# Kernel tuning notes

Hardware: AMD Instinct MI355X
Metric: run time of the kernel (lower is better)

The kernel has to match this reference:

```python
import jax, jax.numpy as jnp
import numpy as np

N_NODES = 100000
N_EDGES = 1600000
D = 128          # in_dim == out_dim
H = 8            # num_heads
DH = D // H      # head dim = 16
DFF = 2 * D
EPS_LN = 1e-5


def _ln(x, g, b):
    mu = jnp.mean(x, axis=-1, keepdims=True)
    var = jnp.var(x, axis=-1, keepdims=True)
    return (x - mu) * jax.lax.rsqrt(var + EPS_LN) * g + b


def setup_inputs() -> dict:
    key = jax.random.key(0)
    ks = jax.random.split(key, 12)
    s = 1.0 / np.sqrt(D)
    inp = {
        "h": jax.random.normal(ks[0], (N_NODES, D), jnp.float32),
        "src": jax.random.randint(ks[1], (N_EDGES,), 0, N_NODES, jnp.int32),
        "dst": jax.random.randint(ks[2], (N_EDGES,), 0, N_NODES, jnp.int32),
        "Wq": jax.random.normal(ks[3], (D, D), jnp.float32) * s,
        "Wk": jax.random.normal(ks[4], (D, D), jnp.float32) * s,
        "Wv": jax.random.normal(ks[5], (D, D), jnp.float32) * s,
        "Wo": jax.random.normal(ks[6], (D, D), jnp.float32) * s,
        "bo": jnp.zeros((D,), jnp.float32),
        "ln1_g": jnp.ones((D,), jnp.float32),
        "ln1_b": jnp.zeros((D,), jnp.float32),
        "W1": jax.random.normal(ks[7], (D, DFF), jnp.float32) * s,
        "b1": jnp.zeros((DFF,), jnp.float32),
        "W2": jax.random.normal(ks[8], (DFF, D), jnp.float32) * (1.0 / np.sqrt(DFF)),
        "b2": jnp.zeros((D,), jnp.float32),
        "ln2_g": jnp.ones((D,), jnp.float32),
        "ln2_b": jnp.zeros((D,), jnp.float32),
    }
    return inp


def reference(h, src, dst, Wq, Wk, Wv, Wo, bo, ln1_g, ln1_b, W1, b1, W2, b2, ln2_g, ln2_b):
    n = h.shape[0]
    # Q/K/V projections (no bias), split into heads: [N, H, DH]
    Q = (h @ Wq).reshape(n, H, DH)
    K = (h @ Wk).reshape(n, H, DH)
    V = (h @ Wv).reshape(n, H, DH)

    # edge-wise attention score: K[src] . Q[dst] / sqrt(DH), exp-clamped
    score = jnp.einsum("ehd,ehd->eh", K[src], Q[dst]) / np.sqrt(DH)  # [E, H]
    score = jnp.exp(jnp.clip(score, -5.0, 5.0))

    # weighted message sum + normalizer via segment reduce over dst
    m = V[src] * score[:, :, None]                                   # [E, H, DH]
    wV = jax.ops.segment_sum(m, dst, num_segments=n)                 # [N, H, DH]
    z = jax.ops.segment_sum(score, dst, num_segments=n)              # [N, H]

    h_attn = (wV / (z[:, :, None] + 1e-6)).reshape(n, D)

    # output projection + residual + LN
    x = h + (h_attn @ Wo + bo)
    x = _ln(x, ln1_g, ln1_b)

    # FFN + residual + LN
    y = jax.nn.relu(x @ W1 + b1) @ W2 + b2
    x = _ln(x + y, ln2_g, ln2_b)
    return x
```

## Files before the change

### kernel.cpp

```cpp
#include <hip/hip_runtime.h>
#include <hip/hip_bf16.h>
#include <math.h>


typedef __attribute__((ext_vector_type(8))) short bf16x8;
typedef __attribute__((ext_vector_type(4))) float f32x4;

#define BSHIFT 9
#define BSIZE  512

template<int K, bool AF32, bool RELU, bool LN, bool RESID, bool BIAS, bool YW>
__global__ __launch_bounds__(256)
void gemm_mfma(const void* __restrict__ Ap, int lda,
               const __hip_bfloat16* __restrict__ Bt, int ldbt,
               const float* __restrict__ bias, const float* __restrict__ resid,
               const float* __restrict__ lng, const float* __restrict__ lnb,
               float* __restrict__ Cf, __hip_bfloat16* __restrict__ Cb, int ldc,
               size_t bt_ystride, size_t cb_ystride, int N)
{
    constexpr int CK = 128;
    __shared__ unsigned short As[64 * 136];
    __shared__ unsigned short Bs[128 * 136];

    const int tid  = threadIdx.x;
    const int row0 = blockIdx.x * 64;
    int col0 = 0;
    if (YW) { Bt += blockIdx.y * bt_ystride; Cb += blockIdx.y * cb_ystride; }
    else    col0 = blockIdx.y * 128;

    const int wave = tid >> 6, lane = tid & 63;
    const int quad = lane >> 4, l15 = lane & 15;

    f32x4 acc[8];
    #pragma unroll
    for (int t = 0; t < 8; ++t) acc[t] = (f32x4)0.f;

    for (int kc = 0; kc < K; kc += CK) {
        #pragma unroll
        for (int it = 0; it < 4; ++it) {
            int i = tid + it * 256;
            int r = i >> 4, kb = i & 15;
            int rg = row0 + r; if (rg > N - 1) rg = N - 1;
            if (AF32) {
                const float* Af = (const float*)Ap;
                const float4 f0 = *(const float4*)&Af[(size_t)rg * lda + kc + kb * 8];
                const float4 f1 = *(const float4*)&Af[(size_t)rg * lda + kc + kb * 8 + 4];
                __hip_bfloat162 b01 = __float22bfloat162_rn(make_float2(f0.x, f0.y));
                __hip_bfloat162 b23 = __float22bfloat162_rn(make_float2(f0.z, f0.w));
                __hip_bfloat162 b45 = __float22bfloat162_rn(make_float2(f1.x, f1.y));
                __hip_bfloat162 b67 = __float22bfloat162_rn(make_float2(f1.z, f1.w));
                uint4 u;
                u.x = *(unsigned*)&b01; u.y = *(unsigned*)&b23;
                u.z = *(unsigned*)&b45; u.w = *(unsigned*)&b67;
                *(uint4*)&As[r * 136 + kb * 8] = u;
            } else {
                const __hip_bfloat16* Ab = (const __hip_bfloat16*)Ap;
                *(uint4*)&As[r * 136 + kb * 8] =
                    *(const uint4*)&Ab[(size_t)rg * lda + kc + kb * 8];
            }
        }
        #pragma unroll
        for (int it = 0; it < 8; ++it) {
            int i = tid + it * 256;
            int r = i >> 4, kb = i & 15;
            *(uint4*)&Bs[r * 136 + kb * 8] =
                *(const uint4*)&Bt[(size_t)(col0 + r) * ldbt + kc + kb * 8];
        }
        __syncthreads();
        const unsigned short* ap = &As[(wave * 16 + l15) * 136 + quad * 8];
        const unsigned short* bp = &Bs[l15 * 136 + quad * 8];
        #pragma unroll
        for (int ks = 0; ks < 4; ++ks) {
            bf16x8 a = *(const bf16x8*)(ap + ks * 32);
            #pragma unroll
            for (int t = 0; t < 8; ++t) {
                bf16x8 b = *(const bf16x8*)(bp + t * 16 * 136 + ks * 32);
                acc[t] = __builtin_amdgcn_mfma_f32_16x16x32_bf16(a, b, acc[t], 0, 0, 0);
            }
        }
        __syncthreads();
    }

    const int rbase = row0 + wave * 16 + quad * 4;

    float vals[8][4];
    #pragma unroll
    for (int t = 0; t < 8; ++t) {
        float bv = BIAS ? bias[col0 + t * 16 + l15] : 0.f;
        #pragma unroll
        for (int i = 0; i < 4; ++i) vals[t][i] = acc[t][i] + bv;
    }
    if (RESID) {
        #pragma unroll
        for (int i = 0; i < 4; ++i) {
            int row = rbase + i;
            if (row < N) {
                #pragma unroll
                for (int t = 0; t < 8; ++t)
                    vals[t][i] += resid[(size_t)row * 128 + t * 16 + l15];
            }
        }
    }
    if (RELU) {
        #pragma unroll
        for (int t = 0; t < 8; ++t)
            #pragma unroll
            for (int i = 0; i < 4; ++i) vals[t][i] = fmaxf(vals[t][i], 0.f);
    }
    if (LN) {
        #pragma unroll
        for (int i = 0; i < 4; ++i) {
            float s = 0.f, sq = 0.f;
            #pragma unroll
            for (int t = 0; t < 8; ++t) { float v = vals[t][i]; s += v; sq += v * v; }
            s  += __shfl_xor(s, 1);  s  += __shfl_xor(s, 2);
            s  += __shfl_xor(s, 4);  s  += __shfl_xor(s, 8);
            sq += __shfl_xor(sq, 1); sq += __shfl_xor(sq, 2);
            sq += __shfl_xor(sq, 4); sq += __shfl_xor(sq, 8);
            float m  = s * (1.f / 128.f);
            float rs = rsqrtf(sq * (1.f / 128.f) - m * m + 1e-5f);
            #pragma unroll
            for (int t = 0; t < 8; ++t) {
                float g = lng[t * 16 + l15], b = lnb[t * 16 + l15];
                vals[t][i] = (vals[t][i] - m) * rs * g + b;
            }
        }
    }
    #pragma unroll
    for (int i = 0; i < 4; ++i) {
        int row = rbase + i;
        if (row >= N) continue;
        if (Cf) {
            #pragma unroll
            for (int t = 0; t < 8; ++t)
                Cf[(size_t)row * ldc + col0 + t * 16 + l15] = vals[t][i];
        }
        if (Cb) {
            #pragma unroll
            for (int t = 0; t < 8; ++t)
                Cb[(size_t)row * ldc + col0 + t * 16 + l15] = __float2bfloat16(vals[t][i]);
        }
    }
}

struct WArgs {
    const float* src[6];
    __hip_bfloat16* dst[6];
    int R[6], C[6];
};
__global__ __launch_bounds__(256)
void cast_w(WArgs wa)
{
    int w = blockIdx.y;
    int R = wa.R[w], C = wa.C[w];
    int i = blockIdx.x * 256 + threadIdx.x;
    if (i >= R * C) return;
    int sh = (C == 256) ? 8 : 7;
    int r = i >> sh, c = i & (C - 1);
    wa.dst[w][(size_t)c * R + r] = __float2bfloat16(wa.src[w][i]);
}


__global__ __launch_bounds__(256)
void bucket_hist(const int* __restrict__ dst, int* __restrict__ bCnt,
                 int E, int chunk, int NB)
{
    __shared__ int bh[256];
    const int t = threadIdx.x;
    bh[t] = 0;
    __syncthreads();
    const int s0 = blockIdx.x * chunk;
    const int s1 = min(E, s0 + chunk);
    for (int i = s0 + t; i < s1; i += 256)
        atomicAdd(&bh[dst[i] >> BSHIFT], 1);
    __syncthreads();
    if (t < NB && bh[t]) atomicAdd(&bCnt[t], bh[t]);
}

__global__ __launch_bounds__(256)
void bucket_scan(const int* __restrict__ bCnt, int* __restrict__ bBase,
                 int* __restrict__ gCur, int* __restrict__ rowStart,
                 int N, int E, int NB)
{
    __shared__ int wsum[4];
    const int t = threadIdx.x, lane = t & 63, wv = t >> 6;
    int v = (t < NB) ? bCnt[t] : 0;
    const int s = v;
    for (int off = 1; off < 64; off <<= 1) {
        int u = __shfl_up(v, off);
        if (lane >= off) v += u;
    }
    if (lane == 63) wsum[wv] = v;
    __syncthreads();
    int add = 0;
    for (int w = 0; w < wv; ++w) add += wsum[w];
    const int excl = v + add - s;
    if (t <= NB) bBase[t] = excl;
    if (t < NB)  gCur[t]  = excl;
    if (t == 0)  rowStart[N] = E;
}

__global__ __launch_bounds__(256)
void partition_kernel(const int* __restrict__ src, const int* __restrict__ dst,
                      int* __restrict__ gCur, uint2* __restrict__ P,
                      int E, int chunk, int NB)
{
    __shared__ int ch[256];
    __shared__ int cur[256];
    const int t = threadIdx.x;
    ch[t] = 0;
    __syncthreads();
    const int s0 = blockIdx.x * chunk;
    const int s1 = min(E, s0 + chunk);
    for (int i = s0 + t; i < s1; i += 256)
        atomicAdd(&ch[dst[i] >> BSHIFT], 1);
    __syncthreads();
    if (t < NB) {
        int c = ch[t];
        cur[t] = c ? atomicAdd(&gCur[t], c) : 0;
    }
    __syncthreads();
    for (int i = s0 + t; i < s1; i += 256) {
        int d = dst[i];
        int pos = atomicAdd(&cur[d >> BSHIFT], 1);
        P[pos] = make_uint2((unsigned)src[i], (unsigned)d);
    }
}

__global__ __launch_bounds__(256)
void bucket_scatter(const uint2* __restrict__ P, const int* __restrict__ bBase,
                    int* __restrict__ rowStart, int* __restrict__ esrc, int N)
{
    __shared__ int hist[BSIZE];
    __shared__ int cur[BSIZE];
    __shared__ int wsum[4];

    const int b  = blockIdx.x;
    const int t  = threadIdx.x;
    const int d0 = b << BSHIFT;
    const int bb  = bBase[b];
    const int cnt = bBase[b + 1] - bb;

    hist[t] = 0; hist[t + 256] = 0;
    __syncthreads();
    for (int i = t; i < cnt; i += 256)
        atomicAdd(&hist[(int)P[bb + i].y - d0], 1);
    __syncthreads();

    {
        const int a0 = hist[2 * t], a1 = hist[2 * t + 1];
        int v = a0 + a1;
        const int s = v;
        const int lane = t & 63, wv = t >> 6;
        for (int off = 1; off < 64; off <<= 1) {
            int u = __shfl_up(v, off);
            if (lane >= off) v += u;
        }
        if (lane == 63) wsum[wv] = v;
        __syncthreads();
        int add = 0;
        for (int w = 0; w < wv; ++w) add += wsum[w];
        const int exclT = v + add - s;
        cur[2 * t]     = exclT;
        cur[2 * t + 1] = exclT + a0;
    }
    __syncthreads();
    for (int i = t; i < BSIZE; i += 256) {
        int d = d0 + i;
        if (d < N) rowStart[d] = bb + cur[i];
    }
    __syncthreads();
    for (int i = t; i < cnt; i += 256) {
        uint2 p = P[bb + i];
        int pos = atomicAdd(&cur[(int)p.y - d0], 1);
        esrc[bb + pos] = (int)p.x;
    }
}

__global__ __launch_bounds__(256)
void aggregate_kernel(__hip_bfloat16* __restrict__ Q,
                      const __hip_bfloat16* __restrict__ Km,
                      const __hip_bfloat16* __restrict__ V,
                      const int* __restrict__ esrc,
                      const int* __restrict__ rowStart, int N)
{
    const int lane = threadIdx.x & 63;
    const int wid  = threadIdx.x >> 6;
    const int d    = blockIdx.x * 4 + wid;
    if (d >= N) return;

    const int l5   = lane & 31;
    const int half = lane >> 5;

    const uint2* K2 = (const uint2*)Km;
    const uint2* V2 = (const uint2*)V;
    uint2*       Q2 = (uint2*)Q;

    const uint2 qraw = Q2[(unsigned)d * 32u + (unsigned)l5];
    const float q0 = __uint_as_float(qraw.x << 16);
    const float q1 = __uint_as_float(qraw.x & 0xffff0000u);
    const float q2 = __uint_as_float(qraw.y << 16);
    const float q3 = __uint_as_float(qraw.y & 0xffff0000u);

    const int beg = rowStart[d];
    const int end = rowStart[d + 1];

    float a0 = 0.f, a1 = 0.f, a2 = 0.f, a3 = 0.f, zacc = 0.f;
    const float S = 0.36067376022224085f;
    const float C = 7.2134752044448170f;

    for (int base = beg; base < end; base += 64) {
        int n = end - base; if (n > 64) n = 64;
        int mysrc = (lane < n) ? esrc[base + lane] : 0;
        const int nf = n >> 1;
        int bidx = half;
        for (int j = 0; j < nf; ++j, bidx += 2) {
            const int s = __shfl(mysrc, bidx);
            const unsigned off = (unsigned)s * 32u + (unsigned)l5;
            const uint2 kraw = K2[off];
            const uint2 vraw = V2[off];
            float p = __uint_as_float(kraw.x << 16)         * q0
                    + __uint_as_float(kraw.x & 0xffff0000u) * q1
                    + __uint_as_float(kraw.y << 16)         * q2
                    + __uint_as_float(kraw.y & 0xffff0000u) * q3;
            p += __shfl_xor(p, 1);
            p += __shfl_xor(p, 2);
            const float tt = fminf(C, fmaxf(-C, p * S));
            const float se = exp2f(tt);
            a0 += __uint_as_float(vraw.x << 16)         * se;
            a1 += __uint_as_float(vraw.x & 0xffff0000u) * se;
            a2 += __uint_as_float(vraw.y << 16)         * se;
            a3 += __uint_as_float(vraw.y & 0xffff0000u) * se;
            zacc += se;
        }
        if (n & 1) {
            const int s = __shfl(mysrc, n - 1);
            const unsigned off = (unsigned)s * 32u + (unsigned)l5;
            const uint2 kraw = K2[off];
            const uint2 vraw = V2[off];
            float p = __uint_as_float(kraw.x << 16)         * q0
                    + __uint_as_float(kraw.x & 0xffff0000u) * q1
                    + __uint_as_float(kraw.y << 16)         * q2
                    + __uint_as_float(kraw.y & 0xffff0000u) * q3;
            p += __shfl_xor(p, 1);
            p += __shfl_xor(p, 2);
            const float tt = fminf(C, fmaxf(-C, p * S));
            float se = exp2f(tt);
            se = half ? 0.f : se;
            a0 += __uint_as_float(vraw.x << 16)         * se;
            a1 += __uint_as_float(vraw.x & 0xffff0000u) * se;
            a2 += __uint_as_float(vraw.y << 16)         * se;
            a3 += __uint_as_float(vraw.y & 0xffff0000u) * se;
            zacc += se;
        }
    }

    a0 += __shfl_xor(a0, 32); a1 += __shfl_xor(a1, 32);
    a2 += __shfl_xor(a2, 32); a3 += __shfl_xor(a3, 32);
    zacc += __shfl_xor(zacc, 32);

    if (half == 0) {
        const float inv = 1.0f / (zacc + 1e-6f);
        __hip_bfloat162 p0 = __float22bfloat162_rn(make_float2(a0 * inv, a1 * inv));
        __hip_bfloat162 p1 = __float22bfloat162_rn(make_float2(a2 * inv, a3 * inv));
        uint2 o;
        o.x = *(unsigned*)&p0;
        o.y = *(unsigned*)&p1;
        Q2[(unsigned)d * 32u + (unsigned)l5] = o;
    }
}

extern "C" void kernel_launch(void* const* d_in, const int* in_sizes, int n_in,
                              void* d_out, int out_size, void* d_ws, size_t ws_size,
                              hipStream_t stream)
{
    const float* h    = (const float*)d_in[0];
    const int*   src  = (const int*)  d_in[1];
    const int*   dst  = (const int*)  d_in[2];
    const float* Wq   = (const float*)d_in[3];
    const float* Wk   = (const float*)d_in[4];
    const float* Wv   = (const float*)d_in[5];
    const float* Wo   = (const float*)d_in[6];
    const float* bo   = (const float*)d_in[7];
    const float* ln1g = (const float*)d_in[8];
    const float* ln1b = (const float*)d_in[9];
    const float* W1   = (const float*)d_in[10];
    const float* b1   = (const float*)d_in[11];
    const float* W2   = (const float*)d_in[12];
    const float* b2   = (const float*)d_in[13];
    const float* ln2g = (const float*)d_in[14];
    const float* ln2b = (const float*)d_in[15];

    const int N = in_sizes[0] / 128;
    const int E = in_sizes[1];
    const int NB = (N + BSIZE - 1) >> BSHIFT;

    __hip_bfloat16* Qh = (__hip_bfloat16*)d_ws;
    __hip_bfloat16* Kh = Qh + (size_t)N * 128;
    __hip_bfloat16* Vh = Kh + (size_t)N * 128;
    __hip_bfloat16* Xh = Vh + (size_t)N * 128;
    float*          Xf = (float*)(Xh + (size_t)N * 128);
    __hip_bfloat16* Wt = (__hip_bfloat16*)(Xf + (size_t)N * 128);
    __hip_bfloat16* Wqt = Wt;
    __hip_bfloat16* Wkt = Wqt + 16384;
    __hip_bfloat16* Wvt = Wkt + 16384;
    __hip_bfloat16* Wot = Wvt + 16384;
    __hip_bfloat16* W1t = Wot + 16384;
    __hip_bfloat16* W2t = W1t + 32768;
    int* ib       = (int*)(W2t + 32768);
    int* bCnt     = ib;
    int* bBase    = ib + 256;
    int* gCur     = ib + 514;
    int* rowStart = ib + 770;
    int* esrc     = ib + 770 + N + 2;
    uint2* P      = (uint2*)Xf;
    __hip_bfloat16* Th = Qh;

    const dim3 blk(256);
    const int  nb    = (N + 63) / 64;
    const int  chunk = (E + 255) / 256;

    WArgs wa;
    wa.src[0] = Wq; wa.src[1] = Wk; wa.src[2] = Wv; wa.src[3] = Wo; wa.src[4] = W1; wa.src[5] = W2;
    wa.dst[0] = Wqt; wa.dst[1] = Wkt; wa.dst[2] = Wvt; wa.dst[3] = Wot; wa.dst[4] = W1t; wa.dst[5] = W2t;
    wa.R[0] = wa.R[1] = wa.R[2] = wa.R[3] = 128; wa.R[4] = 128; wa.R[5] = 256;
    wa.C[0] = wa.C[1] = wa.C[2] = wa.C[3] = 128; wa.C[4] = 256; wa.C[5] = 128;
    cast_w<<<dim3(128, 6), blk, 0, stream>>>(wa);

    gemm_mfma<128,true,false,false,false,false,true><<<dim3(nb, 3), blk, 0, stream>>>(
        h, 128, Wqt, 128, nullptr, nullptr, nullptr, nullptr,
        nullptr, Qh, 128, (size_t)16384, (size_t)N * 128, N);

    hipMemsetAsync(bCnt, 0, 256 * sizeof(int), stream);
    bucket_hist<<<dim3(256), blk, 0, stream>>>(dst, bCnt, E, chunk, NB);
    bucket_scan<<<dim3(1), blk, 0, stream>>>(bCnt, bBase, gCur, rowStart, N, E, NB);
    partition_kernel<<<dim3(256), blk, 0, stream>>>(src, dst, gCur, P, E, chunk, NB);
    bucket_scatter<<<dim3(NB), blk, 0, stream>>>(P, bBase, rowStart, esrc, N);

    aggregate_kernel<<<dim3((N + 3) / 4), blk, 0, stream>>>(Qh, Kh, Vh, esrc, rowStart, N);

    gemm_mfma<128,false,false,true,true,true,false><<<dim3(nb, 1), blk, 0, stream>>>(
        Qh, 128, Wot, 128, bo, h, ln1g, ln1b, Xf, Xh, 128, 0, 0, N);

    gemm_mfma<128,false,true,false,false,true,false><<<dim3(nb, 2), blk, 0, stream>>>(
        Xh, 128, W1t, 128, b1, nullptr, nullptr, nullptr, nullptr, Th, 256, 0, 0, N);

    gemm_mfma<256,false,false,true,true,true,false><<<dim3(nb, 1), blk, 0, stream>>>(
        Th, 256, W2t, 256, b2, Xf, ln2g, ln2b, (float*)d_out, nullptr, 128, 0, 0, N);
}
```

Measured before the change: 421.9 us.

## Interleave K and V rows, use fp16 Q/K with fdot2 in aggregation

K and V projections are written into one interleaved buffer (512 bytes per node), so each edge gather reads K and V from the same row. Q and K are now stored as fp16, which lets the dot product use packed fdot2 instructions. Each lane handles 8 channels through 16-byte loads, and a wave processes four edges at once instead of two. The single fused QKV GEMM launch becomes three separate launches, and fp16 Q/K adds some range and precision risk.

```diff
diff --git a/kernel.cpp b/kernel.cpp
--- a/kernel.cpp
+++ b/kernel.cpp
@@ -5,11 +5,22 @@
 
 typedef __attribute__((ext_vector_type(8))) short bf16x8;
 typedef __attribute__((ext_vector_type(4))) float f32x4;
+typedef __attribute__((ext_vector_type(2))) _Float16 half2_t;
 
 #define BSHIFT 9
 #define BSIZE  512
 
-template<int K, bool AF32, bool RELU, bool LN, bool RESID, bool BIAS, bool YW>
+static __device__ __forceinline__ half2_t h2(unsigned u) {
+    return __builtin_bit_cast(half2_t, u);
+}
+static __device__ __forceinline__ float bl(unsigned u) {
+    return __uint_as_float(u << 16);
+}
+static __device__ __forceinline__ float bh(unsigned u) {
+    return __uint_as_float(u & 0xffff0000u);
+}
+
+template<int K, bool AF32, bool RELU, bool LN, bool RESID, bool BIAS, bool YW, bool F16O>
 __global__ __launch_bounds__(256)
 void gemm_mfma(const void* __restrict__ Ap, int lda,
                const __hip_bfloat16* __restrict__ Bt, int ldbt,
@@ -137,8 +148,14 @@
         }
         if (Cb) {
             #pragma unroll
-            for (int t = 0; t < 8; ++t)
-                Cb[(size_t)row * ldc + col0 + t * 16 + l15] = __float2bfloat16(vals[t][i]);
+            for (int t = 0; t < 8; ++t) {
+                if (F16O)
+                    ((_Float16*)Cb)[(size_t)row * ldc + col0 + t * 16 + l15] =
+                        (_Float16)vals[t][i];
+                else
+                    Cb[(size_t)row * ldc + col0 + t * 16 + l15] =
+                        __float2bfloat16(vals[t][i]);
+            }
         }
     }
 }
@@ -159,7 +176,6 @@
     int r = i >> sh, c = i & (C - 1);
     wa.dst[w][(size_t)c * R + r] = __float2bfloat16(wa.src[w][i]);
 }
-
 
 __global__ __launch_bounds__(256)
 void bucket_hist(const int* __restrict__ dst, int* __restrict__ bCnt,
@@ -278,9 +294,8 @@
 }
 
 __global__ __launch_bounds__(256)
-void aggregate_kernel(__hip_bfloat16* __restrict__ Q,
-                      const __hip_bfloat16* __restrict__ Km,
-                      const __hip_bfloat16* __restrict__ V,
+void aggregate_kernel(unsigned short* __restrict__ Qp,
+                      const unsigned short* __restrict__ KV,
                       const int* __restrict__ esrc,
                       const int* __restrict__ rowStart, int N)
 {
@@ -289,84 +304,70 @@
     const int d    = blockIdx.x * 4 + wid;
     if (d >= N) return;
 
-    const int l5   = lane & 31;
-    const int half = lane >> 5;
-
-    const uint2* K2 = (const uint2*)Km;
-    const uint2* V2 = (const uint2*)V;
-    uint2*       Q2 = (uint2*)Q;
-
-    const uint2 qraw = Q2[(unsigned)d * 32u + (unsigned)l5];
-    const float q0 = __uint_as_float(qraw.x << 16);
-    const float q1 = __uint_as_float(qraw.x & 0xffff0000u);
-    const float q2 = __uint_as_float(qraw.y << 16);
-    const float q3 = __uint_as_float(qraw.y & 0xffff0000u);
+    const int c = lane & 15;
+    const int g = lane >> 4;
+
+    const uint4 qraw = *(const uint4*)(Qp + (size_t)d * 128u + c * 8);
+    const half2_t q0 = h2(qraw.x), q1 = h2(qraw.y),
+                  q2 = h2(qraw.z), q3 = h2(qraw.w);
 
     const int beg = rowStart[d];
     const int end = rowStart[d + 1];
 
-    float a0 = 0.f, a1 = 0.f, a2 = 0.f, a3 = 0.f, zacc = 0.f;
+    float a0 = 0.f, a1 = 0.f, a2 = 0.f, a3 = 0.f;
+    float a4 = 0.f, a5 = 0.f, a6 = 0.f, a7 = 0.f, z = 0.f;
     const float S = 0.36067376022224085f;
     const float C = 7.2134752044448170f;
+    const char* KVb = (const char*)KV + (size_t)c * 16;
 
     for (int base = beg; base < end; base += 64) {
         int n = end - base; if (n > 64) n = 64;
-        int mysrc = (lane < n) ? esrc[base + lane] : 0;
-        const int nf = n >> 1;
-        int bidx = half;
-        for (int j = 0; j < nf; ++j, bidx += 2) {
-            const int s = __shfl(mysrc, bidx);
-            const unsigned off = (unsigned)s * 32u + (unsigned)l5;
-            const uint2 kraw = K2[off];
-            const uint2 vraw = V2[off];
-            float p = __uint_as_float(kraw.x << 16)         * q0
-                    + __uint_as_float(kraw.x & 0xffff0000u) * q1
-                    + __uint_as_float(kraw.y << 16)         * q2
-                    + __uint_as_float(kraw.y & 0xffff0000u) * q3;
+        const int mysrc = (lane < n) ? esrc[base + lane] : 0;
+        const int jmax = (n + 3) >> 2;
+        #pragma unroll 2
+        for (int j = 0; j < jmax; ++j) {
+            const int idx = j * 4 + g;
+            const bool valid = idx < n;
+            const int s = __shfl(mysrc, valid ? idx : n - 1);
+            const char* bp = KVb + (size_t)(unsigned)s * 512u;
+            const uint4 kr = *(const uint4*)bp;
+            const uint4 vr = *(const uint4*)(bp + 256);
+            float p = __builtin_amdgcn_fdot2(h2(kr.x), q0, 0.f, false);
+            p = __builtin_amdgcn_fdot2(h2(kr.y), q1, p, false);
+            p = __builtin_amdgcn_fdot2(h2(kr.z), q2, p, false);
+            p = __builtin_amdgcn_fdot2(h2(kr.w), q3, p, false);
             p += __shfl_xor(p, 1);
-            p += __shfl_xor(p, 2);
-            const float tt = fminf(C, fmaxf(-C, p * S));
-            const float se = exp2f(tt);
-            a0 += __uint_as_float(vraw.x << 16)         * se;
-            a1 += __uint_as_float(vraw.x & 0xffff0000u) * se;
-            a2 += __uint_as_float(vraw.y << 16)         * se;
-            a3 += __uint_as_float(vraw.y & 0xffff0000u) * se;
-            zacc += se;
-        }
-        if (n & 1) {
-            const int s = __shfl(mysrc, n - 1);
-            const unsigned off = (unsigned)s * 32u + (unsigned)l5;
-            const uint2 kraw = K2[off];
-            const uint2 vraw = V2[off];
-            float p = __uint_as_float(kraw.x << 16)         * q0
-                    + __uint_as_float(kraw.x & 0xffff0000u) * q1
-                    + __uint_as_float(kraw.y << 16)         * q2
-                    + __uint_as_float(kraw.y & 0xffff0000u) * q3;
-            p += __shfl_xor(p, 1);
-            p += __shfl_xor(p, 2);
-            const float tt = fminf(C, fmaxf(-C, p * S));
-            float se = exp2f(tt);
-            se = half ? 0.f : se;
-            a0 += __uint_as_float(vraw.x << 16)         * se;
-            a1 += __uint_as_float(vraw.x & 0xffff0000u) * se;
-            a2 += __uint_as_float(vraw.y << 16)         * se;
-            a3 += __uint_as_float(vraw.y & 0xffff0000u) * se;
-            zacc += se;
-        }
-    }
-
+            float se = exp2f(fminf(C, fmaxf(-C, p * S)));
+            se = valid ? se : 0.f;
+            a0 += bl(vr.x) * se; a1 += bh(vr.x) * se;
+            a2 += bl(vr.y) * se; a3 += bh(vr.y) * se;
+            a4 += bl(vr.z) * se; a5 += bh(vr.z) * se;
+            a6 += bl(vr.w) * se; a7 += bh(vr.w) * se;
+            z  += se;
+        }
+    }
+
+    a0 += __shfl_xor(a0, 16); a1 += __shfl_xor(a1, 16);
+    a2 += __shfl_xor(a2, 16); a3 += __shfl_xor(a3, 16);
+    a4 += __shfl_xor(a4, 16); a5 += __shfl_xor(a5, 16);
+    a6 += __shfl_xor(a6, 16); a7 += __shfl_xor(a7, 16);
+    z  += __shfl_xor(z, 16);
     a0 += __shfl_xor(a0, 32); a1 += __shfl_xor(a1, 32);
     a2 += __shfl_xor(a2, 32); a3 += __shfl_xor(a3, 32);
-    zacc += __shfl_xor(zacc, 32);
-
-    if (half == 0) {
-        const float inv = 1.0f / (zacc + 1e-6f);
+    a4 += __shfl_xor(a4, 32); a5 += __shfl_xor(a5, 32);
+    a6 += __shfl_xor(a6, 32); a7 += __shfl_xor(a7, 32);
+    z  += __shfl_xor(z, 32);
+
+    if (g == 0) {
+        const float inv = 1.0f / (z + 1e-6f);
         __hip_bfloat162 p0 = __float22bfloat162_rn(make_float2(a0 * inv, a1 * inv));
         __hip_bfloat162 p1 = __float22bfloat162_rn(make_float2(a2 * inv, a3 * inv));
-        uint2 o;
-        o.x = *(unsigned*)&p0;
-        o.y = *(unsigned*)&p1;
-        Q2[(unsigned)d * 32u + (unsigned)l5] = o;
+        __hip_bfloat162 p2 = __float22bfloat162_rn(make_float2(a4 * inv, a5 * inv));
+        __hip_bfloat162 p3 = __float22bfloat162_rn(make_float2(a6 * inv, a7 * inv));
+        uint4 o;
+        o.x = *(unsigned*)&p0; o.y = *(unsigned*)&p1;
+        o.z = *(unsigned*)&p2; o.w = *(unsigned*)&p3;
+        *(uint4*)(Qp + (size_t)d * 128u + c * 8) = o;
     }
 }
 
@@ -395,10 +396,9 @@
     const int E = in_sizes[1];
     const int NB = (N + BSIZE - 1) >> BSHIFT;
 
-    __hip_bfloat16* Qh = (__hip_bfloat16*)d_ws;
-    __hip_bfloat16* Kh = Qh + (size_t)N * 128;
-    __hip_bfloat16* Vh = Kh + (size_t)N * 128;
-    __hip_bfloat16* Xh = Vh + (size_t)N * 128;
+    unsigned short* Qh = (unsigned short*)d_ws;
+    unsigned short* KV = Qh + (size_t)N * 128;
+    __hip_bfloat16* Xh = (__hip_bfloat16*)(KV + (size_t)N * 256);
     float*          Xf = (float*)(Xh + (size_t)N * 128);
     __hip_bfloat16* Wt = (__hip_bfloat16*)(Xf + (size_t)N * 128);
     __hip_bfloat16* Wqt = Wt;
@@ -414,7 +414,7 @@
     int* rowStart = ib + 770;
     int* esrc     = ib + 770 + N + 2;
     uint2* P      = (uint2*)Xf;
-    __hip_bfloat16* Th = Qh;
+    __hip_bfloat16* Th = (__hip_bfloat16*)KV;
 
     const dim3 blk(256);
     const int  nb    = (N + 63) / 64;
@@ -427,9 +427,15 @@
     wa.C[0] = wa.C[1] = wa.C[2] = wa.C[3] = 128; wa.C[4] = 256; wa.C[5] = 128;
     cast_w<<<dim3(128, 6), blk, 0, stream>>>(wa);
 
-    gemm_mfma<128,true,false,false,false,false,true><<<dim3(nb, 3), blk, 0, stream>>>(
+    gemm_mfma<128,true,false,false,false,false,false,true><<<dim3(nb, 1), blk, 0, stream>>>(
         h, 128, Wqt, 128, nullptr, nullptr, nullptr, nullptr,
-        nullptr, Qh, 128, (size_t)16384, (size_t)N * 128, N);
+        nullptr, (__hip_bfloat16*)Qh, 128, 0, 0, N);
+    gemm_mfma<128,true,false,false,false,false,false,true><<<dim3(nb, 1), blk, 0, stream>>>(
+        h, 128, Wkt, 128, nullptr, nullptr, nullptr, nullptr,
+        nullptr, (__hip_bfloat16*)KV, 256, 0, 0, N);
+    gemm_mfma<128,true,false,false,false,false,false,false><<<dim3(nb, 1), blk, 0, stream>>>(
+        h, 128, Wvt, 128, nullptr, nullptr, nullptr, nullptr,
+        nullptr, (__hip_bfloat16*)(KV + 128), 256, 0, 0, N);
 
     hipMemsetAsync(bCnt, 0, 256 * sizeof(int), stream);
     bucket_hist<<<dim3(256), blk, 0, stream>>>(dst, bCnt, E, chunk, NB);
@@ -437,14 +443,14 @@
     partition_kernel<<<dim3(256), blk, 0, stream>>>(src, dst, gCur, P, E, chunk, NB);
     bucket_scatter<<<dim3(NB), blk, 0, stream>>>(P, bBase, rowStart, esrc, N);
 
-    aggregate_kernel<<<dim3((N + 3) / 4), blk, 0, stream>>>(Qh, Kh, Vh, esrc, rowStart, N);
-
-    gemm_mfma<128,false,false,true,true,true,false><<<dim3(nb, 1), blk, 0, stream>>>(
-        Qh, 128, Wot, 128, bo, h, ln1g, ln1b, Xf, Xh, 128, 0, 0, N);
-
-    gemm_mfma<128,false,true,false,false,true,false><<<dim3(nb, 2), blk, 0, stream>>>(
+    aggregate_kernel<<<dim3((N + 3) / 4), blk, 0, stream>>>(Qh, KV, esrc, rowStart, N);
+
+    gemm_mfma<128,false,false,true,true,true,false,false><<<dim3(nb, 1), blk, 0, stream>>>(
+        (__hip_bfloat16*)Qh, 128, Wot, 128, bo, h, ln1g, ln1b, Xf, Xh, 128, 0, 0, N);
+
+    gemm_mfma<128,false,true,false,false,true,false,false><<<dim3(nb, 2), blk, 0, stream>>>(
         Xh, 128, W1t, 128, b1, nullptr, nullptr, nullptr, nullptr, Th, 256, 0, 0, N);
 
-    gemm_mfma<256,false,false,true,true,true,false><<<dim3(nb, 1), blk, 0, stream>>>(
+    gemm_mfma<256,false,false,true,true,true,false,false><<<dim3(nb, 1), blk, 0, stream>>>(
         Th, 256, W2t, 256, b2, Xf, ln2g, ln2b, (float*)d_out, nullptr, 128, 0, 0, N);
 }
```

New measurement: 431.8 us. +2.4%, slower.
